# Kernel optimization log

Hardware: AMD Instinct MI355X
Metric: run time of the kernel (lower is better)

## Reference

```python
import jax, jax.numpy as jnp
import numpy as np

LRELU_GAIN = np.sqrt(2.0).astype(np.float32)  # apply_activation gain for leaky_relu


def setup_inputs() -> dict:
    key = jax.random.key(0)
    ks = jax.random.split(key, 8)
    N, H, W, C_in = 8, 256, 256, 128
    num_ws, w_dim, fmaps, kernel = 16, 512, 128, 3
    return {
        "x": jax.random.normal(ks[0], (N, H, W, C_in), dtype=jnp.float32),
        "dlatents": jax.random.normal(ks[1], (N, num_ws, w_dim), dtype=jnp.float32),
        "noise": jax.random.normal(ks[2], (N, H, W, 1), dtype=jnp.float32),
        "affine_w": jax.random.normal(ks[3], (w_dim, C_in), dtype=jnp.float32),
        "affine_b": jnp.ones((C_in,), dtype=jnp.float32),  # bias_init=1
        "conv_w": jax.random.normal(ks[4], (kernel, kernel, C_in, fmaps), dtype=jnp.float32),
        "conv_b": jax.random.normal(ks[5], (fmaps,), dtype=jnp.float32),
        "noise_strength": jax.random.uniform(ks[6], (1,), dtype=jnp.float32),
        "layer_idx": 5,
    }


def reference(x, dlatents, noise, affine_w, affine_b, conv_w, conv_b, noise_strength, layer_idx):
    # --- affine (equalized-lr Linear, lr_multiplier=1): s = z @ (W/sqrt(fan_in)) + b ---
    w_dim = affine_w.shape[0]
    z = dlatents[:, layer_idx]                                   # [N, w_dim]
    s = z @ (affine_w * np.float32(1.0 / np.sqrt(w_dim))) + affine_b   # [N, C_in]

    # --- equalized-lr conv weight: w * 1/sqrt(k*k*C_in) ---
    k, _, cin, cout = conv_w.shape
    w = conv_w * np.float32(1.0 / np.sqrt(k * k * cin))          # [k,k,Cin,Cout]

    # --- demodulation coefficient d[n,o] = rsqrt(sum_{k,k,i} (w*s)^2 + eps) ---
    d = jax.lax.rsqrt(jnp.einsum('hwio,ni->no', jnp.square(w), jnp.square(s)) + 1e-8)  # [N, Cout]

    # --- non-fused modconv: modulate input, shared conv, demodulate output ---
    xm = x * s[:, None, None, :]                                 # [N,H,W,Cin]
    y = jax.lax.conv_general_dilated(
        xm, w, window_strides=(1, 1), padding='SAME',
        dimension_numbers=('NHWC', 'HWIO', 'NHWC'))              # [N,H,W,Cout]
    y = y * d[:, None, None, :]

    # --- noise injection, bias, activation (leaky_relu 0.2 with sqrt(2) gain) ---
    y = y + noise_strength[0] * noise
    y = y + conv_b
    return jax.nn.leaky_relu(y, negative_slope=0.2) * LRELU_GAIN
```

## Files before the change

kernel.cpp:

```cpp
#include <hip/hip_runtime.h>

typedef unsigned short u16;
typedef unsigned int   u32;
typedef __bf16 v8bf __attribute__((ext_vector_type(8)));
typedef float  v4f  __attribute__((ext_vector_type(4)));

#define INV_SQRT_W   0.044194173824159216f
#define INV_SQRT_KKC 0.029462782549439483f
#define LRELU_GAIN   1.4142135623730951f

__device__ __forceinline__ u16 f2bf(float f) {
    u32 u = __float_as_uint(f);
    u = (u + 0x7fffu + ((u >> 16) & 1u)) >> 16;
    return (u16)u;
}

__global__ void k_s(const float* __restrict__ dlat,
                    const float* __restrict__ aw,
                    const float* __restrict__ ab,
                    const int*   __restrict__ lidx,
                    float* __restrict__ s_out)
{
    const int n   = blockIdx.x;
    const int tid = threadIdx.x;
    const int i   = tid & 127, kh = tid >> 7;
    const int li  = lidx[0];
    const float* z = dlat + (n * 16 + li) * 512 + kh * 256;
    const float* a = aw + kh * 256 * 128 + i;
    float a0 = 0.f, a1 = 0.f, a2 = 0.f, a3 = 0.f;
    for (int k = 0; k < 256; k += 4) {
        a0 += z[k + 0] * a[(k + 0) * 128];
        a1 += z[k + 1] * a[(k + 1) * 128];
        a2 += z[k + 2] * a[(k + 2) * 128];
        a3 += z[k + 3] * a[(k + 3) * 128];
    }
    __shared__ float part[256];
    part[tid] = a0 + a1 + a2 + a3;
    __syncthreads();
    if (tid < 128)
        s_out[n * 128 + i] = (part[i] + part[i + 128]) * INV_SQRT_W + ab[i];
}

__global__ void k_w2(const float* __restrict__ cw, float* __restrict__ W2)
{
    const int idx = blockIdx.x * 256 + threadIdx.x;
    float acc = 0.f;
    #pragma unroll
    for (int t = 0; t < 9; ++t) {
        float w = cw[t * 16384 + idx];
        acc += w * w;
    }
    W2[idx] = acc * (INV_SQRT_KKC * INV_SQRT_KKC);
}

__global__ void k_d(const float* __restrict__ W2,
                    const float* __restrict__ s_buf,
                    float* __restrict__ d_out)
{
    const int n = blockIdx.x;
    const int o = threadIdx.x;
    __shared__ float s2[128];
    float sv = s_buf[n * 128 + o];
    s2[o] = sv * sv;
    __syncthreads();
    float acc = 1e-8f;
    #pragma unroll 4
    for (int i = 0; i < 128; ++i)
        acc += W2[i * 128 + o] * s2[i];
    d_out[n * 128 + o] = 1.0f / sqrtf(acc);
}

__global__ void k_wmod(const float* __restrict__ cw,
                       const float* __restrict__ s_buf,
                       const float* __restrict__ d_buf,
                       u16* __restrict__ wmod)
{
    const int b   = blockIdx.x;
    const int n   = b / 36;
    const int s   = b - n * 36;
    const int ph  = s / 18;
    const int r   = s - ph * 18;
    const int q2  = r / 9;
    const int rr  = r - q2 * 9;
    const int tw  = rr / 3, th = rr - tw * 3;
    const int tap = th * 3 + tw;
    const int cibase = ph * 64 + q2 * 32;
    const int tid = threadIdx.x;
    __shared__ float ssh[32], dsh[128];
    if (tid < 32)  ssh[tid] = s_buf[n * 128 + cibase + tid] * INV_SQRT_KKC;
    if (tid < 128) dsh[tid] = d_buf[n * 128 + tid];
    __syncthreads();
    u16* wt = wmod + ((size_t)b << 12);
    #pragma unroll
    for (int rep = 0; rep < 2; ++rep) {
        int t2   = rep * 256 + tid;
        int g    = t2 >> 7;
        int cout = t2 & 127;
        float dv = dsh[cout];
        u32 pk[4];
        #pragma unroll
        for (int jj = 0; jj < 4; ++jj) {
            int cl = g * 8 + jj * 2;
            float v0 = cw[((tap * 128 + cibase + cl) << 7) + cout]     * ssh[cl]     * dv;
            float v1 = cw[((tap * 128 + cibase + cl + 1) << 7) + cout] * ssh[cl + 1] * dv;
            pk[jj] = (u32)f2bf(v0) | ((u32)f2bf(v1) << 16);
        }
        *(uint4*)&wt[(g << 10) + (cout << 3)] = *(uint4*)pk;
    }
}

template<int T>
__device__ __forceinline__ void conv_step(const u16* __restrict__ bp,
                                          const u16* a_base,
                                          v8bf af[10], v8bf bfP[3][4],
                                          v4f acc[8][4])
{
    constexpr int q2 = T / 9, rr = T % 9, tw = rr / 3, th = rr % 3;
    constexpr int slot = T % 3;
    if constexpr (th == 0) {
        #pragma unroll
        for (int r = 0; r < 10; ++r)
            af[r] = *(const v8bf*)(a_base + q2 * 10400 + r * 144 + tw * 8);
    }
    #pragma unroll
    for (int mi = 0; mi < 8; ++mi)
        #pragma unroll
        for (int ni = 0; ni < 4; ++ni)
            acc[mi][ni] = __builtin_amdgcn_mfma_f32_16x16x32_bf16(
                af[mi + th], bfP[slot][ni], acc[mi][ni], 0, 0, 0);
    if constexpr (T + 3 < 18) {
        #pragma unroll
        for (int ni = 0; ni < 4; ++ni)
            bfP[slot][ni] = *(const v8bf*)(bp + (T + 3) * 4096 + ni * 128);
    }
}

__global__ __launch_bounds__(256, 2) void k_conv(
    const float* __restrict__ x,
    const float* __restrict__ noise,
    const float* __restrict__ conv_b,
    const float* __restrict__ nstr,
    const u16*   __restrict__ wmod,
    float* __restrict__ out)
{
    __shared__ __align__(16) u16 xs[20800];

    const int bid0 = blockIdx.x;
    const int bid  = ((bid0 & 7) << 8) + (bid0 >> 3);
    const int n  = bid >> 8;
    const int hb = (bid >> 4) & 15;
    const int wb = bid & 15;
    const int h0 = hb << 4, w0 = wb << 4;

    const int tid  = threadIdx.x;
    const int lane = tid & 63;
    const int wid  = tid >> 6;
    const int wm   = wid >> 1;
    const int wq   = wid & 1;
    const int lr   = lane & 15;
    const int kg   = lane >> 4;

    const float* xbase = x + ((size_t)n << 16) * 128;

    #define STAGE_X(ph)                                                              \
    for (int t = tid; t < 2592; t += 256) {                                          \
        int q = t >> 3, g = t & 7;                                                   \
        int rr_ = q / 18, cc = q - rr_ * 18;                                         \
        int gh = h0 + rr_ - 1, gw = w0 + cc - 1;                                     \
        float v0=0.f,v1=0.f,v2=0.f,v3=0.f,v4=0.f,v5=0.f,v6=0.f,v7=0.f;               \
        if ((unsigned)gh < 256u && (unsigned)gw < 256u) {                            \
            const float* src = xbase + (size_t)((gh << 8) + gw) * 128                \
                               + (ph) * 64 + (g << 3);                               \
            float4 fa = *(const float4*)(src);                                       \
            float4 fb = *(const float4*)(src + 4);                                   \
            v0=fa.x; v1=fa.y; v2=fa.z; v3=fa.w; v4=fb.x; v5=fb.y; v6=fb.z; v7=fb.w;  \
        }                                                                            \
        v8bf pk;                                                                     \
        pk[0]=(__bf16)v0; pk[1]=(__bf16)v1; pk[2]=(__bf16)v2; pk[3]=(__bf16)v3;      \
        pk[4]=(__bf16)v4; pk[5]=(__bf16)v5; pk[6]=(__bf16)v6; pk[7]=(__bf16)v7;      \
        *(v8bf*)&xs[g * 2600 + q * 8] = pk;                                          \
    }

    u16* const a_base = &xs[kg * 2600 + (wm * 144 + lr) * 8];
    const u16* const b_base = wmod + (size_t)n * 147456 + kg * 1024 + (wq * 64 + lr) * 8;

    v4f acc[8][4];
    #pragma unroll
    for (int a = 0; a < 8; ++a)
        #pragma unroll
        for (int b2 = 0; b2 < 4; ++b2) {
            v4f zz = {0.f, 0.f, 0.f, 0.f};
            acc[a][b2] = zz;
        }
    v8bf af[10];
    v8bf bfP[3][4];

    #pragma unroll 1
    for (int ph = 0; ph < 2; ++ph) {
        if (ph) __syncthreads();
        STAGE_X(ph)
        const u16* bp = b_base + ph * 73728;
        #pragma unroll
        for (int t3 = 0; t3 < 3; ++t3)
            #pragma unroll
            for (int ni = 0; ni < 4; ++ni)
                bfP[t3][ni] = *(const v8bf*)(bp + t3 * 4096 + ni * 128);
        __syncthreads();

        conv_step< 0>(bp, a_base, af, bfP, acc);
        conv_step< 1>(bp, a_base, af, bfP, acc);
        conv_step< 2>(bp, a_base, af, bfP, acc);
        conv_step< 3>(bp, a_base, af, bfP, acc);
        conv_step< 4>(bp, a_base, af, bfP, acc);
        conv_step< 5>(bp, a_base, af, bfP, acc);
        conv_step< 6>(bp, a_base, af, bfP, acc);
        conv_step< 7>(bp, a_base, af, bfP, acc);
        conv_step< 8>(bp, a_base, af, bfP, acc);
        conv_step< 9>(bp, a_base, af, bfP, acc);
        conv_step<10>(bp, a_base, af, bfP, acc);
        conv_step<11>(bp, a_base, af, bfP, acc);
        conv_step<12>(bp, a_base, af, bfP, acc);
        conv_step<13>(bp, a_base, af, bfP, acc);
        conv_step<14>(bp, a_base, af, bfP, acc);
        conv_step<15>(bp, a_base, af, bfP, acc);
        conv_step<16>(bp, a_base, af, bfP, acc);
        conv_step<17>(bp, a_base, af, bfP, acc);
    }

    const float ns = nstr[0];
    float cb4[4];
    #pragma unroll
    for (int ni = 0; ni < 4; ++ni)
        cb4[ni] = conv_b[wq * 64 + ni * 16 + lr];
    #pragma unroll
    for (int mi = 0; mi < 8; ++mi) {
        const int h = h0 + wm * 8 + mi;
        #pragma unroll
        for (int j = 0; j < 4; ++j) {
            const int w  = w0 + kg * 4 + j;
            const float nz = noise[((n << 8) + h) * 256 + w] * ns;
            float* orow = out + (size_t)((((n << 8) + h) << 8) + w) * 128;
            #pragma unroll
            for (int ni = 0; ni < 4; ++ni) {
                const int cout = wq * 64 + ni * 16 + lr;
                float v = acc[mi][ni][j] + nz + cb4[ni];
                v = (v < 0.f ? 0.2f * v : v) * LRELU_GAIN;
                orow[cout] = v;
            }
        }
    }
}

extern "C" void kernel_launch(void* const* d_in, const int* in_sizes, int n_in,
                              void* d_out, int out_size, void* d_ws, size_t ws_size,
                              hipStream_t stream) {
    const float* x     = (const float*)d_in[0];
    const float* dlat  = (const float*)d_in[1];
    const float* noise = (const float*)d_in[2];
    const float* aw    = (const float*)d_in[3];
    const float* ab    = (const float*)d_in[4];
    const float* cw    = (const float*)d_in[5];
    const float* cb    = (const float*)d_in[6];
    const float* nstr  = (const float*)d_in[7];
    const int*   lidx  = (const int*)d_in[8];
    float* out = (float*)d_out;

    float* s_buf = (float*)d_ws;
    float* d_buf = (float*)((char*)d_ws + 4096);
    float* W2    = (float*)((char*)d_ws + 8192);
    u16*   wmod  = (u16*)((char*)d_ws + 8192);

    k_w2  <<<64,  256, 0, stream>>>(cw, W2);
    k_s   <<<8,   256, 0, stream>>>(dlat, aw, ab, lidx, s_buf);
    k_d   <<<8,   128, 0, stream>>>(W2, s_buf, d_buf);
    k_wmod<<<288, 256, 0, stream>>>(cw, s_buf, d_buf, wmod);
    k_conv<<<2048,256, 0, stream>>>(x, noise, cb, nstr, wmod, out);
}
```

Before: 225.8 us.

## Halve conv tile height, stage all input channels at once, raise occupancy

The conv tile shrinks from 16x16 to 8x16 output pixels. All 128 input channels are now staged into LDS in one pass instead of two 64-channel phases, which removes the mid-kernel barrier and re-staging. Weight layout is regrouped into four 32-channel k-chunks to match, and the B prefetch depth drops from 3 to 2 so launch bounds can ask for 3 blocks per CU. Smaller tiles double the grid and raise the halo overhead (10 of 8 rows) and the weight reloads per output pixel.

```diff
diff --git a/kernel.cpp b/kernel.cpp
--- a/kernel.cpp
+++ b/kernel.cpp
@@ -78,13 +78,11 @@
     const int b   = blockIdx.x;
     const int n   = b / 36;
     const int s   = b - n * 36;
-    const int ph  = s / 18;
-    const int r   = s - ph * 18;
-    const int q2  = r / 9;
-    const int rr  = r - q2 * 9;
-    const int tw  = rr / 3, th = rr - tw * 3;
+    const int q4  = s / 9;
+    const int r   = s - q4 * 9;
+    const int tw  = r / 3, th = r - tw * 3;
     const int tap = th * 3 + tw;
-    const int cibase = ph * 64 + q2 * 32;
+    const int cibase = q4 * 32;
     const int tid = threadIdx.x;
     __shared__ float ssh[32], dsh[128];
     if (tid < 32)  ssh[tid] = s_buf[n * 128 + cibase + tid] * INV_SQRT_KKC;
@@ -112,30 +110,30 @@
 template<int T>
 __device__ __forceinline__ void conv_step(const u16* __restrict__ bp,
                                           const u16* a_base,
-                                          v8bf af[10], v8bf bfP[3][4],
-                                          v4f acc[8][4])
-{
-    constexpr int q2 = T / 9, rr = T % 9, tw = rr / 3, th = rr % 3;
-    constexpr int slot = T % 3;
+                                          v8bf af[6], v8bf bfP[2][4],
+                                          v4f acc[4][4])
+{
+    constexpr int q4 = T / 9, rr = T % 9, tw = rr / 3, th = rr % 3;
+    constexpr int slot = T & 1;
     if constexpr (th == 0) {
         #pragma unroll
-        for (int r = 0; r < 10; ++r)
-            af[r] = *(const v8bf*)(a_base + q2 * 10400 + r * 144 + tw * 8);
-    }
-    #pragma unroll
-    for (int mi = 0; mi < 8; ++mi)
+        for (int r = 0; r < 6; ++r)
+            af[r] = *(const v8bf*)(a_base + q4 * 5824 + (r * 18 + tw) * 8);
+    }
+    #pragma unroll
+    for (int mi = 0; mi < 4; ++mi)
         #pragma unroll
         for (int ni = 0; ni < 4; ++ni)
             acc[mi][ni] = __builtin_amdgcn_mfma_f32_16x16x32_bf16(
                 af[mi + th], bfP[slot][ni], acc[mi][ni], 0, 0, 0);
-    if constexpr (T + 3 < 18) {
+    if constexpr (T + 2 < 36) {
         #pragma unroll
         for (int ni = 0; ni < 4; ++ni)
-            bfP[slot][ni] = *(const v8bf*)(bp + (T + 3) * 4096 + ni * 128);
-    }
-}
-
-__global__ __launch_bounds__(256, 2) void k_conv(
+            bfP[slot][ni] = *(const v8bf*)(bp + (T + 2) * 4096 + ni * 128);
+    }
+}
+
+__global__ __launch_bounds__(256, 3) void k_conv(
     const float* __restrict__ x,
     const float* __restrict__ noise,
     const float* __restrict__ conv_b,
@@ -143,14 +141,14 @@
     const u16*   __restrict__ wmod,
     float* __restrict__ out)
 {
-    __shared__ __align__(16) u16 xs[20800];
+    __shared__ __align__(16) u16 xs[23296];
 
     const int bid0 = blockIdx.x;
-    const int bid  = ((bid0 & 7) << 8) + (bid0 >> 3);
-    const int n  = bid >> 8;
-    const int hb = (bid >> 4) & 15;
+    const int bid  = ((bid0 & 7) << 9) + (bid0 >> 3);
+    const int n  = bid >> 9;
+    const int hb = (bid >> 4) & 31;
     const int wb = bid & 15;
-    const int h0 = hb << 4, w0 = wb << 4;
+    const int h0 = hb << 3, w0 = wb << 4;
 
     const int tid  = threadIdx.x;
     const int lane = tid & 63;
@@ -161,71 +159,82 @@
     const int kg   = lane >> 4;
 
     const float* xbase = x + ((size_t)n << 16) * 128;
-
-    #define STAGE_X(ph)                                                              \
-    for (int t = tid; t < 2592; t += 256) {                                          \
-        int q = t >> 3, g = t & 7;                                                   \
-        int rr_ = q / 18, cc = q - rr_ * 18;                                         \
-        int gh = h0 + rr_ - 1, gw = w0 + cc - 1;                                     \
-        float v0=0.f,v1=0.f,v2=0.f,v3=0.f,v4=0.f,v5=0.f,v6=0.f,v7=0.f;               \
-        if ((unsigned)gh < 256u && (unsigned)gw < 256u) {                            \
-            const float* src = xbase + (size_t)((gh << 8) + gw) * 128                \
-                               + (ph) * 64 + (g << 3);                               \
-            float4 fa = *(const float4*)(src);                                       \
-            float4 fb = *(const float4*)(src + 4);                                   \
-            v0=fa.x; v1=fa.y; v2=fa.z; v3=fa.w; v4=fb.x; v5=fb.y; v6=fb.z; v7=fb.w;  \
-        }                                                                            \
-        v8bf pk;                                                                     \
-        pk[0]=(__bf16)v0; pk[1]=(__bf16)v1; pk[2]=(__bf16)v2; pk[3]=(__bf16)v3;      \
-        pk[4]=(__bf16)v4; pk[5]=(__bf16)v5; pk[6]=(__bf16)v6; pk[7]=(__bf16)v7;      \
-        *(v8bf*)&xs[g * 2600 + q * 8] = pk;                                          \
-    }
-
-    u16* const a_base = &xs[kg * 2600 + (wm * 144 + lr) * 8];
     const u16* const b_base = wmod + (size_t)n * 147456 + kg * 1024 + (wq * 64 + lr) * 8;
 
-    v4f acc[8][4];
-    #pragma unroll
-    for (int a = 0; a < 8; ++a)
+    v8bf bfP[2][4];
+    #pragma unroll
+    for (int t2 = 0; t2 < 2; ++t2)
+        #pragma unroll
+        for (int ni = 0; ni < 4; ++ni)
+            bfP[t2][ni] = *(const v8bf*)(b_base + t2 * 4096 + ni * 128);
+
+    for (int t = tid; t < 2880; t += 256) {
+        int g = t & 15, q = t >> 4;
+        int rr_ = q / 18, cc = q - rr_ * 18;
+        int gh = h0 + rr_ - 1, gw = w0 + cc - 1;
+        float v0=0.f,v1=0.f,v2=0.f,v3=0.f,v4=0.f,v5=0.f,v6=0.f,v7=0.f;
+        if ((unsigned)gh < 256u && (unsigned)gw < 256u) {
+            const float* src = xbase + (size_t)((gh << 8) + gw) * 128 + (g << 3);
+            float4 fa = *(const float4*)(src);
+            float4 fb = *(const float4*)(src + 4);
+            v0=fa.x; v1=fa.y; v2=fa.z; v3=fa.w; v4=fb.x; v5=fb.y; v6=fb.z; v7=fb.w;
+        }
+        v8bf pk;
+        pk[0]=(__bf16)v0; pk[1]=(__bf16)v1; pk[2]=(__bf16)v2; pk[3]=(__bf16)v3;
+        pk[4]=(__bf16)v4; pk[5]=(__bf16)v5; pk[6]=(__bf16)v6; pk[7]=(__bf16)v7;
+        *(v8bf*)&xs[g * 1456 + q * 8] = pk;
+    }
+
+    v4f acc[4][4];
+    #pragma unroll
+    for (int a = 0; a < 4; ++a)
         #pragma unroll
         for (int b2 = 0; b2 < 4; ++b2) {
             v4f zz = {0.f, 0.f, 0.f, 0.f};
             acc[a][b2] = zz;
         }
-    v8bf af[10];
-    v8bf bfP[3][4];
-
-    #pragma unroll 1
-    for (int ph = 0; ph < 2; ++ph) {
-        if (ph) __syncthreads();
-        STAGE_X(ph)
-        const u16* bp = b_base + ph * 73728;
-        #pragma unroll
-        for (int t3 = 0; t3 < 3; ++t3)
-            #pragma unroll
-            for (int ni = 0; ni < 4; ++ni)
-                bfP[t3][ni] = *(const v8bf*)(bp + t3 * 4096 + ni * 128);
-        __syncthreads();
-
-        conv_step< 0>(bp, a_base, af, bfP, acc);
-        conv_step< 1>(bp, a_base, af, bfP, acc);
-        conv_step< 2>(bp, a_base, af, bfP, acc);
-        conv_step< 3>(bp, a_base, af, bfP, acc);
-        conv_step< 4>(bp, a_base, af, bfP, acc);
-        conv_step< 5>(bp, a_base, af, bfP, acc);
-        conv_step< 6>(bp, a_base, af, bfP, acc);
-        conv_step< 7>(bp, a_base, af, bfP, acc);
-        conv_step< 8>(bp, a_base, af, bfP, acc);
-        conv_step< 9>(bp, a_base, af, bfP, acc);
-        conv_step<10>(bp, a_base, af, bfP, acc);
-        conv_step<11>(bp, a_base, af, bfP, acc);
-        conv_step<12>(bp, a_base, af, bfP, acc);
-        conv_step<13>(bp, a_base, af, bfP, acc);
-        conv_step<14>(bp, a_base, af, bfP, acc);
-        conv_step<15>(bp, a_base, af, bfP, acc);
-        conv_step<16>(bp, a_base, af, bfP, acc);
-        conv_step<17>(bp, a_base, af, bfP, acc);
-    }
+
+    const u16* const a_base = &xs[kg * 1456 + (wm * 72 + lr) * 8];
+
+    __syncthreads();
+
+    v8bf af[6];
+    conv_step< 0>(b_base, a_base, af, bfP, acc);
+    conv_step< 1>(b_base, a_base, af, bfP, acc);
+    conv_step< 2>(b_base, a_base, af, bfP, acc);
+    conv_step< 3>(b_base, a_base, af, bfP, acc);
+    conv_step< 4>(b_base, a_base, af, bfP, acc);
+    conv_step< 5>(b_base, a_base, af, bfP, acc);
+    conv_step< 6>(b_base, a_base, af, bfP, acc);
+    conv_step< 7>(b_base, a_base, af, bfP, acc);
+    conv_step< 8>(b_base, a_base, af, bfP, acc);
+    conv_step< 9>(b_base, a_base, af, bfP, acc);
+    conv_step<10>(b_base, a_base, af, bfP, acc);
+    conv_step<11>(b_base, a_base, af, bfP, acc);
+    conv_step<12>(b_base, a_base, af, bfP, acc);
+    conv_step<13>(b_base, a_base, af, bfP, acc);
+    conv_step<14>(b_base, a_base, af, bfP, acc);
+    conv_step<15>(b_base, a_base, af, bfP, acc);
+    conv_step<16>(b_base, a_base, af, bfP, acc);
+    conv_step<17>(b_base, a_base, af, bfP, acc);
+    conv_step<18>(b_base, a_base, af, bfP, acc);
+    conv_step<19>(b_base, a_base, af, bfP, acc);
+    conv_step<20>(b_base, a_base, af, bfP, acc);
+    conv_step<21>(b_base, a_base, af, bfP, acc);
+    conv_step<22>(b_base, a_base, af, bfP, acc);
+    conv_step<23>(b_base, a_base, af, bfP, acc);
+    conv_step<24>(b_base, a_base, af, bfP, acc);
+    conv_step<25>(b_base, a_base, af, bfP, acc);
+    conv_step<26>(b_base, a_base, af, bfP, acc);
+    conv_step<27>(b_base, a_base, af, bfP, acc);
+    conv_step<28>(b_base, a_base, af, bfP, acc);
+    conv_step<29>(b_base, a_base, af, bfP, acc);
+    conv_step<30>(b_base, a_base, af, bfP, acc);
+    conv_step<31>(b_base, a_base, af, bfP, acc);
+    conv_step<32>(b_base, a_base, af, bfP, acc);
+    conv_step<33>(b_base, a_base, af, bfP, acc);
+    conv_step<34>(b_base, a_base, af, bfP, acc);
+    conv_step<35>(b_base, a_base, af, bfP, acc);
 
     const float ns = nstr[0];
     float cb4[4];
@@ -233,8 +242,8 @@
     for (int ni = 0; ni < 4; ++ni)
         cb4[ni] = conv_b[wq * 64 + ni * 16 + lr];
     #pragma unroll
-    for (int mi = 0; mi < 8; ++mi) {
-        const int h = h0 + wm * 8 + mi;
+    for (int mi = 0; mi < 4; ++mi) {
+        const int h = h0 + wm * 4 + mi;
         #pragma unroll
         for (int j = 0; j < 4; ++j) {
             const int w  = w0 + kg * 4 + j;
@@ -274,5 +283,5 @@
     k_s   <<<8,   256, 0, stream>>>(dlat, aw, ab, lidx, s_buf);
     k_d   <<<8,   128, 0, stream>>>(W2, s_buf, d_buf);
     k_wmod<<<288, 256, 0, stream>>>(cw, s_buf, d_buf, wmod);
-    k_conv<<<2048,256, 0, stream>>>(x, noise, cb, nstr, wmod, out);
-}
+    k_conv<<<4096,256, 0, stream>>>(x, noise, cb, nstr, wmod, out);
+}
```

After: 225.5 us. About the same (-0.1%).
